# Kernel tuning notes

Measured on AMD Instinct MI355X. Metric: run time of the kernel, lower is better.

The kernel has to match this reference:

```python
import jax, jax.numpy as jnp
from jax import lax
import numpy as np

EPS = 1e-6
D_KQ = 256  # per-head q/k dim; softmax scale = sqrt(256) = 16


def layernorm(x, g, b):
    m = jnp.mean(x, axis=-1, keepdims=True)
    v = jnp.var(x, axis=-1, keepdims=True)  # biased, matches torch LayerNorm
    return (x - m) / jnp.sqrt(v + EPS) * g + b


def lrelu(t):
    return jnp.where(t > 0, t, 0.1 * t)


def setup_inputs() -> dict:
    key = jax.random.key(0)
    ks = jax.random.split(key, 10)
    B, C, H, W = 256, 17, 84, 84
    d_model, heads = 512, 4
    hid = D_KQ * heads  # 1024
    out_dim = 256
    s = 0.05
    return {
        "x": jax.random.normal(ks[0], (B, C, H, W), jnp.float32),
        "conv1_w": jax.random.normal(ks[1], (64, C, 8, 8), jnp.float32) * s,
        "conv1_b": jnp.zeros((64,), jnp.float32),
        "conv2_w": jax.random.normal(ks[2], (510, 64, 4, 4), jnp.float32) * s,
        "conv2_b": jnp.zeros((510,), jnp.float32),
        "wq": jax.random.normal(ks[3], (hid, d_model), jnp.float32) * s,
        "wk": jax.random.normal(ks[4], (hid, d_model), jnp.float32) * s,
        "wv": jax.random.normal(ks[5], (hid, d_model), jnp.float32) * s,
        "ln_e_g": jnp.ones((hid,), jnp.float32),
        "ln_e_b": jnp.zeros((hid,), jnp.float32),
        "wo": jax.random.normal(ks[6], (d_model, hid), jnp.float32) * s,
        "ln_g": jnp.ones((d_model,), jnp.float32),
        "ln_b": jnp.zeros((d_model,), jnp.float32),
        "map_w": jax.random.normal(ks[7], (out_dim, d_model), jnp.float32) * s,
        "map_b": jnp.zeros((out_dim,), jnp.float32),
    }


def reference(x, conv1_w, conv1_b, conv2_w, conv2_b, wq, wk, wv,
              ln_e_g, ln_e_b, wo, ln_g, ln_b, map_w, map_b):
    dn = ("NCHW", "OIHW", "NCHW")
    # feature extractor
    y = lax.conv_general_dilated(x, conv1_w, (4, 4), "VALID", dimension_numbers=dn)
    y = lrelu(y + conv1_b[None, :, None, None])
    y = lax.conv_general_dilated(y, conv2_w, (2, 2), "VALID", dimension_numbers=dn)
    y = lrelu(y + conv2_b[None, :, None, None])  # [B,510,H2,W2]
    B, Cc, H2, W2 = y.shape
    N = H2 * W2
    e = jnp.transpose(y.reshape(B, Cc, N), (0, 2, 1))  # [B,N,510]
    # coordinate augmentation: [(i//W)/H, (i%W)/W]
    idx = jnp.arange(N)
    coord = jnp.stack([(idx // W2) / H2, (idx % W2) / W2], axis=-1).astype(e.dtype)
    e = jnp.concatenate([e, jnp.broadcast_to(coord, (B, N, 2))], axis=-1)  # [B,N,512]
    heads = 4
    # projections + per-projection LayerNorm over full hid dim (pre-head-split)
    q = layernorm(e @ wq.T, ln_e_g, ln_e_b).reshape(B, N, heads, D_KQ)
    k = layernorm(e @ wk.T, ln_e_g, ln_e_b).reshape(B, N, heads, D_KQ)
    v = layernorm(e @ wv.T, ln_e_g, ln_e_b).reshape(B, N, heads, D_KQ)
    scores = jnp.einsum("bnhd,bmhd->bhnm", q, k) / jnp.sqrt(jnp.float32(D_KQ))
    w = jax.nn.softmax(scores, axis=-1)
    nv = jnp.einsum("bhnm,bmhd->bnhd", w, v).reshape(B, N, heads * D_KQ)
    out = layernorm(nv @ wo.T + e, ln_g, ln_b)  # residual + LN
    out = jax.nn.relu(out)
    out = jnp.max(out, axis=1)  # maxout over entities -> [B,512]
    return lrelu(out @ map_w.T + map_b)  # mapping -> [B,256]
```

## Files before the change

kernel.cpp:

```cpp
#include <hip/hip_runtime.h>
#include <hip/hip_bf16.h>
#include <math.h>

typedef __hip_bfloat16 bf16;
using f32x4 = __attribute__((ext_vector_type(4))) float;
using s16x8 = __attribute__((ext_vector_type(8))) short;

#define DEV_INLINE __device__ __forceinline__

static constexpr int BB   = 256;
static constexpr int CIN  = 17;
static constexpr int WIN  = 84;
static constexpr int C1   = 64;
static constexpr int W1   = 20;
static constexpr int P1   = W1 * W1;
static constexpr int C2   = 510;
static constexpr int W2   = 9;
static constexpr int NE   = 81;
static constexpr int DM   = 512;
static constexpr int HID  = 1024;
static constexpr int NH   = 4;
static constexpr int DK   = 256;
static constexpr int MR   = BB * NE;
static constexpr int ODIM = 256;
static constexpr int PLANE = WIN * WIN;
static constexpr int QS   = 3 * HID;

DEV_INLINE float lrelu_f(float v) { return v > 0.f ? v : 0.1f * v; }
DEV_INLINE float bf2f(ushort u) { return __uint_as_float((unsigned)u << 16); }
DEV_INLINE short f2bs(float f) { bf16 t = __float2bfloat16(f); return *reinterpret_cast<short*>(&t); }

DEV_INLINE void gll16(const void* g, const void* l) {
    __builtin_amdgcn_global_load_lds(
        (const __attribute__((address_space(1))) unsigned int*)g,
        (__attribute__((address_space(3))) unsigned int*)l, 16, 0, 0);
}
DEV_INLINE f32x4 mfma16(s16x8 a, s16x8 b, f32x4 c) {
    return __builtin_amdgcn_mfma_f32_16x16x32_bf16(a, b, c, 0, 0, 0);
}

__global__ void k_cast4(const float* __restrict__ s, bf16* __restrict__ d, int n4) {
    const int i4 = blockIdx.x * 256 + threadIdx.x;
    if (i4 >= n4) return;
    const size_t i = (size_t)i4 * 4;
    const float4 v = *(const float4*)(s + i);
    short o[4] = { f2bs(v.x), f2bs(v.y), f2bs(v.z), f2bs(v.w) };
    *(ushort4*)(d + i) = *(ushort4*)o;
}
__global__ void k_castw2(const float* __restrict__ s, bf16* __restrict__ d) {
    const int i = blockIdx.x * 256 + threadIdx.x;
    const int n = i >> 10, rem = i & 1023;
    const int khkw = rem >> 6, ic = rem & 63;
    d[i] = (n < C2) ? __float2bfloat16(s[n * 1024 + ic * 16 + khkw])
                    : __float2bfloat16(0.f);
}
__global__ void k_padb2(const float* __restrict__ s, float* __restrict__ d) {
    const int i = blockIdx.x * 256 + threadIdx.x;
    if (i < 512) d[i] = (i < C2) ? s[i] : 0.f;
}
__global__ void k_castqkv(const float* __restrict__ wq, const float* __restrict__ wk,
                          const float* __restrict__ wv, bf16* __restrict__ d) {
    const int i4 = blockIdx.x * 256 + threadIdx.x;
    const size_t i = (size_t)i4 * 4;
    const int n = (int)(i >> 9), c = (int)(i & 511);
    const float* src = (n < 1024) ? wq : (n < 2048) ? wk : wv;
    const int r = n & 1023;
    const float4 v = *(const float4*)(src + (size_t)r * 512 + c);
    short o[4] = { f2bs(v.x), f2bs(v.y), f2bs(v.z), f2bs(v.w) };
    *(ushort4*)(d + i) = *(ushort4*)o;
}

__global__ __launch_bounds__(512, 1) void k_conv1_mfma(const float* __restrict__ x,
        const bf16* __restrict__ w1b, const float* __restrict__ bias,
        bf16* __restrict__ y1t) {
    __shared__ __align__(16) char pl[2][28224];
    const int b = blockIdx.x;
    const int tid = threadIdx.x;
    const int w = tid >> 6, l = tid & 63;
    const int l15 = l & 15, l4 = l >> 4;
    const float* xb = x + (size_t)b * CIN * PLANE;

    int baseA[4], tval[4];
    #pragma unroll
    for (int j = 0; j < 4; ++j) {
        const int t = w + 8 * j; tval[j] = t;
        int p = t * 16 + l15; if (t >= 25) p = 0;
        const int oh = p / 20, ow = p % 20;
        baseA[j] = (oh * 4 + l4) * 336 + ow * 16;
    }
    float bias_r[4];
    #pragma unroll
    for (int nt = 0; nt < 4; ++nt) bias_r[nt] = bias[nt * 16 + l15];

    #pragma unroll
    for (int it = 0; it < 4; ++it) {
        const int g = it * 512 + tid;
        if (g < 1764) gll16(xb + (size_t)g * 4, pl[0] + (size_t)g * 16);
    }
    __syncthreads();

    f32x4 acc[4][4] = {};
    int cur = 0;
    for (int ic = 0; ic < CIN; ++ic) {
        if (ic + 1 < CIN) {
            const float* src = xb + (size_t)(ic + 1) * PLANE;
            #pragma unroll
            for (int it = 0; it < 4; ++it) {
                const int g = it * 512 + tid;
                if (g < 1764) gll16(src + (size_t)g * 4, pl[cur ^ 1] + (size_t)g * 16);
            }
        }
        s16x8 bq[4][2];
        #pragma unroll
        for (int nt = 0; nt < 4; ++nt)
            #pragma unroll
            for (int ks = 0; ks < 2; ++ks)
                bq[nt][ks] = *(const s16x8*)(w1b + (size_t)(nt * 16 + l15) * 1088
                                             + ic * 64 + (ks * 4 + l4) * 8);
        const char* P = pl[cur];
        #pragma unroll
        for (int j = 0; j < 4; ++j) {
            if (tval[j] < 25) {
                #pragma unroll
                for (int ks = 0; ks < 2; ++ks) {
                    const float* fp = (const float*)(P + baseA[j] + ks * 1344);
                    const f32x4 f0 = *(const f32x4*)fp;
                    const f32x4 f1 = *(const f32x4*)(fp + 4);
                    s16x8 af;
                    #pragma unroll
                    for (int jj = 0; jj < 4; ++jj) {
                        af[jj]     = f2bs(f0[jj]);
                        af[jj + 4] = f2bs(f1[jj]);
                    }
                    #pragma unroll
                    for (int nt = 0; nt < 4; ++nt)
                        acc[j][nt] = mfma16(af, bq[nt][ks], acc[j][nt]);
                }
            }
        }
        __syncthreads();
        cur ^= 1;
    }
    #pragma unroll
    for (int j = 0; j < 4; ++j) {
        if (tval[j] < 25) {
            #pragma unroll
            for (int nt = 0; nt < 4; ++nt) {
                #pragma unroll
                for (int q = 0; q < 4; ++q) {
                    const int pix = tval[j] * 16 + l4 * 4 + q;
                    const int oc  = nt * 16 + l15;
                    y1t[((size_t)b * P1 + pix) * 64 + oc] =
                        __float2bfloat16(lrelu_f(acc[j][nt][q] + bias_r[nt]));
                }
            }
        }
    }
}

__global__ __launch_bounds__(256) void k_gemm_conv2(const bf16* __restrict__ A,
        const bf16* __restrict__ B, const float* __restrict__ bias,
        bf16* __restrict__ Cb) {
    __shared__ __align__(16) char Asm[2][128 * 64];
    __shared__ __align__(16) char Bsm[2][128 * 64];
    const int tid = threadIdx.x;
    const int m0 = blockIdx.y * 128, n0 = blockIdx.x * 128;
    const int w = tid >> 6, l = tid & 63;
    const int wm = w >> 1, wn = w & 1;
    const int l15 = l & 15, l4 = l >> 4;
    const int r0 = tid >> 2, p0 = tid & 3;
    const int r1 = 64 + r0;
    const int sw0 = (p0 ^ ((r0 >> 1) & 3)) << 3;
    const int sw1 = (p0 ^ ((r1 >> 1) & 3)) << 3;
    int bimg[2], ohh[2], oww[2];
    #pragma unroll
    for (int it = 0; it < 2; ++it) {
        const int m = m0 + (it ? r1 : r0);
        bimg[it] = m / 81;
        const int n = m - bimg[it] * 81;
        ohh[it] = n / 9; oww[it] = n - ohh[it] * 9;
    }
    auto stage = [&](int buf, int k0) {
        const int khkw = k0 >> 6, icb = k0 & 63;
        const int kh = khkw >> 2, kwv = khkw & 3;
        const int pix0 = (ohh[0] * 2 + kh) * 20 + oww[0] * 2 + kwv;
        const int pix1 = (ohh[1] * 2 + kh) * 20 + oww[1] * 2 + kwv;
        gll16(A + ((size_t)bimg[0] * P1 + pix0) * 64 + icb + sw0, Asm[buf] + tid * 16);
        gll16(A + ((size_t)bimg[1] * P1 + pix1) * 64 + icb + sw1, Asm[buf] + (256 + tid) * 16);
        gll16(B + (size_t)(n0 + r0) * HID + k0 + sw0, Bsm[buf] + tid * 16);
        gll16(B + (size_t)(n0 + r1) * HID + k0 + sw1, Bsm[buf] + (256 + tid) * 16);
    };
    stage(0, 0);
    __syncthreads();
    f32x4 acc[4][4] = {};
    int cur = 0;
    for (int t = 0; t < 32; ++t) {
        if (t < 31) stage(cur ^ 1, (t + 1) * 32);
        s16x8 af[4], bfv[4];
        #pragma unroll
        for (int i = 0; i < 4; ++i) {
            const int ra = wm * 64 + i * 16 + l15;
            af[i]  = *(const s16x8*)(Asm[cur] + ra * 64 + ((l4 ^ ((ra >> 1) & 3)) << 4));
            const int rb = wn * 64 + i * 16 + l15;
            bfv[i] = *(const s16x8*)(Bsm[cur] + rb * 64 + ((l4 ^ ((rb >> 1) & 3)) << 4));
        }
        #pragma unroll
        for (int i = 0; i < 4; ++i)
            #pragma unroll
            for (int j = 0; j < 4; ++j)
                acc[i][j] = mfma16(af[i], bfv[j], acc[i][j]);
        __syncthreads();
        cur ^= 1;
    }
    #pragma unroll
    for (int i = 0; i < 4; ++i) {
        #pragma unroll
        for (int j = 0; j < 4; ++j) {
            const int col = n0 + wn * 64 + j * 16 + l15;
            #pragma unroll
            for (int q = 0; q < 4; ++q) {
                const int row = m0 + wm * 64 + i * 16 + l4 * 4 + q;
                float v = lrelu_f(acc[i][j][q] + bias[col]);
                if (col >= 510) {
                    const int n = row % 81;
                    v = (col == 510) ? (float)(n / 9) * (1.f / 9.f)
                                     : (float)(n % 9) * (1.f / 9.f);
                }
                Cb[(size_t)row * DM + col] = __float2bfloat16(v);
            }
        }
    }
}

template <int RESID>
__global__ __launch_bounds__(256) void k_gemm_stats(const bf16* __restrict__ A,
        const bf16* __restrict__ B, const bf16* __restrict__ resid,
        bf16* __restrict__ Cb, float2* __restrict__ part,
        int K, int ldc, int nPH) {
    __shared__ __align__(16) char Asm[2][16384];
    __shared__ __align__(16) char Bsm[2][16384];
    const int tid = threadIdx.x;
    const int m0 = blockIdx.y * 128, n0 = blockIdx.x * 128;
    const int w = tid >> 6, l = tid & 63;
    const int wm = w >> 1, wn = w & 1;
    const int l15 = l & 15, l4 = l >> 4;

    auto stage = [&](int buf, int k0) {
        #pragma unroll
        for (int it = 0; it < 4; ++it) {
            const int g = it * 256 + tid;
            const int r = g >> 3, p = g & 7;
            const int sw = (p ^ (r & 7)) << 3;
            gll16(A + (size_t)(m0 + r) * K + k0 + sw, Asm[buf] + g * 16);
            gll16(B + (size_t)(n0 + r) * K + k0 + sw, Bsm[buf] + g * 16);
        }
    };
    stage(0, 0);
    __syncthreads();
    f32x4 acc[4][4] = {};
    int cur = 0;
    const int nt = K >> 6;
    for (int t = 0; t < nt; ++t) {
        if (t + 1 < nt) stage(cur ^ 1, (t + 1) * 64);
        #pragma unroll
        for (int kk = 0; kk < 2; ++kk) {
            s16x8 af[4], bfv[4];
            const int pz = kk * 4 + l4;
            #pragma unroll
            for (int i = 0; i < 4; ++i) {
                const int ra = wm * 64 + i * 16 + l15;
                af[i]  = *(const s16x8*)(Asm[cur] + ra * 128 + ((pz ^ (ra & 7)) << 4));
                const int rb = wn * 64 + i * 16 + l15;
                bfv[i] = *(const s16x8*)(Bsm[cur] + rb * 128 + ((pz ^ (rb & 7)) << 4));
            }
            #pragma unroll
            for (int i = 0; i < 4; ++i)
                #pragma unroll
                for (int j = 0; j < 4; ++j)
                    acc[i][j] = mfma16(af[i], bfv[j], acc[i][j]);
        }
        __syncthreads();
        cur ^= 1;
    }
    #pragma unroll
    for (int i = 0; i < 4; ++i) {
        #pragma unroll
        for (int q = 0; q < 4; ++q) {
            const int row = m0 + wm * 64 + i * 16 + l4 * 4 + q;
            if (RESID) {
                const bf16* rr = resid + (size_t)row * ldc;
                #pragma unroll
                for (int j = 0; j < 4; ++j)
                    acc[i][j][q] += bf2f(*(const ushort*)(rr + n0 + wn * 64 + j * 16 + l15));
            }
            float s = 0.f, s2 = 0.f;
            #pragma unroll
            for (int j = 0; j < 4; ++j) {
                const float v = acc[i][j][q];
                s += v; s2 += v * v;
            }
            #pragma unroll
            for (int o = 1; o < 16; o <<= 1) {
                s  += __shfl_xor(s, o, 64);
                s2 += __shfl_xor(s2, o, 64);
            }
            if (l15 == 0)
                part[(size_t)row * nPH + (n0 >> 6) + wn] = make_float2(s, s2);
            bf16* cr = Cb + (size_t)row * ldc + n0 + wn * 64;
            #pragma unroll
            for (int j = 0; j < 4; ++j)
                cr[j * 16 + l15] = __float2bfloat16(acc[i][j][q]);
        }
    }
}

__global__ void k_red(const float2* __restrict__ part, float2* __restrict__ stats,
                      int total, int nPH, int groups, float invD) {
    const int gid = blockIdx.x * 256 + threadIdx.x;
    if (gid >= total) return;
    const int proj = gid / MR, row = gid - proj * MR;
    const float2* p = part + (size_t)row * (nPH * groups) + proj * nPH;
    float s = 0.f, s2 = 0.f;
    for (int h = 0; h < nPH; ++h) { s += p[h].x; s2 += p[h].y; }
    const float mean = s * invD;
    const float var  = s2 * invD - mean * mean;
    stats[gid] = make_float2(mean, rsqrtf(var + 1e-6f));
}

__global__ __launch_bounds__(256) void k_vt(const bf16* __restrict__ qkv3,
        const float2* __restrict__ vstats, const float* __restrict__ g,
        const float* __restrict__ bprm, bf16* __restrict__ vt) {
    __shared__ bf16 T[81 * 264];
    const int tid = threadIdx.x;
    const int bh = blockIdx.x;
    const int b = bh >> 2, h = bh & 3;
    const int brow = b * NE;
    const int hoff = h * DK;
    for (int gidx = tid; gidx < 81 * 32; gidx += 256) {
        const int m = gidx >> 5, c8 = gidx & 31;
        const int row = brow + m;
        const s16x8 vv = *(const s16x8*)(qkv3 + (size_t)row * QS + 2048 + hoff + c8 * 8);
        const float2 st = vstats[row];
        const int col0 = hoff + c8 * 8;
        const float4 g0 = *(const float4*)(g + col0), g1 = *(const float4*)(g + col0 + 4);
        const float4 b0 = *(const float4*)(bprm + col0), b1 = *(const float4*)(bprm + col0 + 4);
        const float ga[8] = { g0.x, g0.y, g0.z, g0.w, g1.x, g1.y, g1.z, g1.w };
        const float ba[8] = { b0.x, b0.y, b0.z, b0.w, b1.x, b1.y, b1.z, b1.w };
        short o[8];
        #pragma unroll
        for (int jj = 0; jj < 8; ++jj) {
            const float a = st.y * ga[jj];
            o[jj] = f2bs(bf2f((ushort)vv[jj]) * a + (ba[jj] - st.x * a));
        }
        *(s16x8*)(T + m * 264 + c8 * 8) = *(s16x8*)o;
    }
    __syncthreads();
    const int d = tid;
    bf16 row[96];
    #pragma unroll
    for (int m = 0; m < 81; ++m) row[m] = T[m * 264 + d];
    #pragma unroll
    for (int m = 81; m < 96; ++m) row[m] = __float2bfloat16(0.f);
    bf16* out = vt + ((size_t)bh * DK + d) * 96;
    #pragma unroll
    for (int g8 = 0; g8 < 12; ++g8)
        *(s16x8*)(out + g8 * 8) = *(const s16x8*)(&row[g8 * 8]);
}

__global__ __launch_bounds__(512) void k_attn3(const bf16* __restrict__ qkv3,
        const float2* __restrict__ stats, const float* __restrict__ g,
        const float* __restrict__ bprm, const bf16* __restrict__ vt,
        bf16* __restrict__ nv) {
    __shared__ __align__(16) char smem[49152 + 96 * 104 * 2];
    char* Ks = smem;
    bf16* Pb = (bf16*)(smem + 49152);
    const int tid = threadIdx.x;
    const int bh = blockIdx.x;
    const int b = bh >> 2, h = bh & 3;
    const int brow = b * NE;
    const int hoff = h * DK;
    const int w = tid >> 6, l = tid & 63;
    const int l15 = l & 15, l4 = l >> 4;

    for (int gidx = tid; gidx < 96 * 32; gidx += 512) {
        const int r = gidx >> 5, c8 = gidx & 31;
        int krow = brow + r; if (krow >= MR) krow = MR - 1;
        const s16x8 kv = *(const s16x8*)(qkv3 + (size_t)krow * QS + 1024 + hoff + c8 * 8);
        const float2 st = stats[MR + krow];
        const int col0 = hoff + c8 * 8;
        const float4 g0 = *(const float4*)(g + col0), g1 = *(const float4*)(g + col0 + 4);
        const float4 b0 = *(const float4*)(bprm + col0), b1 = *(const float4*)(bprm + col0 + 4);
        const float ga[8] = { g0.x, g0.y, g0.z, g0.w, g1.x, g1.y, g1.z, g1.w };
        const float ba[8] = { b0.x, b0.y, b0.z, b0.w, b1.x, b1.y, b1.z, b1.w };
        short o[8];
        #pragma unroll
        for (int jj = 0; jj < 8; ++jj) {
            const float a = st.y * ga[jj];
            o[jj] = f2bs(bf2f((ushort)kv[jj]) * a + (ba[jj] - st.x * a));
        }
        *(s16x8*)(Ks + r * 512 + ((c8 ^ (r & 7)) << 4)) = *(s16x8*)o;
    }
    __syncthreads();

    if (w < 6) {
        int qrow = brow + w * 16 + l15; if (qrow >= MR) qrow = MR - 1;
        const float2 stq = stats[qrow];
        s16x8 qa[8];
        #pragma unroll
        for (int kk = 0; kk < 8; ++kk) {
            const int col0 = hoff + kk * 32 + l4 * 8;
            const s16x8 qv = *(const s16x8*)(qkv3 + (size_t)qrow * QS + col0);
            const float4 g0 = *(const float4*)(g + col0), g1 = *(const float4*)(g + col0 + 4);
            const float4 b0 = *(const float4*)(bprm + col0), b1 = *(const float4*)(bprm + col0 + 4);
            const float ga[8] = { g0.x, g0.y, g0.z, g0.w, g1.x, g1.y, g1.z, g1.w };
            const float ba[8] = { b0.x, b0.y, b0.z, b0.w, b1.x, b1.y, b1.z, b1.w };
            short o[8];
            #pragma unroll
            for (int jj = 0; jj < 8; ++jj) {
                const float a = stq.y * ga[jj];
                o[jj] = f2bs(bf2f((ushort)qv[jj]) * a + (ba[jj] - stq.x * a));
            }
            qa[kk] = *(s16x8*)o;
        }
        f32x4 sacc[6];
        #pragma unroll
        for (int j = 0; j < 6; ++j) {
            f32x4 a = {};
            const int rb = j * 16 + l15;
            #pragma unroll
            for (int kk = 0; kk < 8; ++kk) {
                const s16x8 kf = *(const s16x8*)(Ks + rb * 512 + (((kk * 4 + l4) ^ (rb & 7)) << 4));
                a = mfma16(qa[kk], kf, a);
            }
            sacc[j] = a;
        }
        float px[6][4];
        #pragma unroll
        for (int q = 0; q < 4; ++q) {
            float m = -1e30f;
            #pragma unroll
            for (int j = 0; j < 6; ++j) {
                const int key = j * 16 + l15;
                const float v = (key < NE) ? sacc[j][q] : -1e30f;
                px[j][q] = v;
                m = fmaxf(m, v);
            }
            #pragma unroll
            for (int o = 1; o < 16; o <<= 1) m = fmaxf(m, __shfl_xor(m, o, 64));
            float s = 0.f;
            #pragma unroll
            for (int j = 0; j < 6; ++j) {
                const float e = __expf((px[j][q] - m) * 0.0625f);
                px[j][q] = e; s += e;
            }
            #pragma unroll
            for (int o = 1; o < 16; o <<= 1) s += __shfl_xor(s, o, 64);
            const float r = 1.f / s;
            #pragma unroll
            for (int j = 0; j < 6; ++j) px[j][q] *= r;
        }
        #pragma unroll
        for (int j = 0; j < 6; ++j)
            #pragma unroll
            for (int q = 0; q < 4; ++q)
                Pb[(w * 16 + l4 * 4 + q) * 104 + j * 16 + l15] =
                    __float2bfloat16(px[j][q]);
    }
    __syncthreads();

    const bf16* vtb = vt + (size_t)bh * DK * 96;
    s16x8 vf[2][3];
    #pragma unroll
    for (int dj = 0; dj < 2; ++dj) {
        const int d = (2 * w + dj) * 16 + l15;
        #pragma unroll
        for (int ks = 0; ks < 3; ++ks)
            vf[dj][ks] = *(const s16x8*)(vtb + (size_t)d * 96 + (ks * 4 + l4) * 8);
    }
    f32x4 oacc[6][2] = {};
    #pragma unroll
    for (int i = 0; i < 6; ++i) {
        s16x8 pa[3];
        #pragma unroll
        for (int ks = 0; ks < 3; ++ks)
            pa[ks] = *(const s16x8*)(Pb + (i * 16 + l15) * 104 + (ks * 4 + l4) * 8);
        #pragma unroll
        for (int dj = 0; dj < 2; ++dj)
            #pragma unroll
            for (int ks = 0; ks < 3; ++ks)
                oacc[i][dj] = mfma16(pa[ks], vf[dj][ks], oacc[i][dj]);
    }
    #pragma unroll
    for (int i = 0; i < 6; ++i) {
        #pragma unroll
        for (int q = 0; q < 4; ++q) {
            const int n = i * 16 + l4 * 4 + q;
            if (n < NE) {
                #pragma unroll
                for (int dj = 0; dj < 2; ++dj) {
                    const int d = (2 * w + dj) * 16 + l15;
                    nv[(size_t)(brow + n) * HID + hoff + d] =
                        __float2bfloat16(oacc[i][dj][q]);
                }
            }
        }
    }
}

__global__ void k_maxpool_ln(const bf16* __restrict__ X, const float2* __restrict__ st,
        const float* __restrict__ g, const float* __restrict__ bprm,
        float* __restrict__ P) {
    const int i = blockIdx.x * 256 + threadIdx.x;
    const int bb = i >> 9, c = i & 511;
    const float gc = g[c], bc = bprm[c];
    const bf16* xp = X + (size_t)bb * NE * DM + c;
    const float2* sp = st + (size_t)bb * NE;
    float mx = -1e30f;
    for (int n = 0; n < NE; ++n) {
        const float2 s = sp[n];
        const float a = s.y * gc;
        const float v = __bfloat162float(xp[(size_t)n * DM]) * a + (bc - s.x * a);
        mx = fmaxf(mx, fmaxf(v, 0.f));
    }
    P[i] = mx;
}

__global__ __launch_bounds__(256) void k_final(const float* __restrict__ P,
        const float* __restrict__ W, const float* __restrict__ bias,
        float* __restrict__ out) {
    const int bb = blockIdx.x;
    __shared__ float pr[DM];
    for (int i = threadIdx.x; i < DM; i += 256) pr[i] = P[(size_t)bb * DM + i];
    __syncthreads();
    const int o = threadIdx.x;
    const float4* w4 = (const float4*)(W + (size_t)o * DM);
    float acc = 0.f;
    for (int c4 = 0; c4 < DM / 4; ++c4) {
        const float4 wv = w4[c4];
        acc += wv.x * pr[c4 * 4] + wv.y * pr[c4 * 4 + 1]
             + wv.z * pr[c4 * 4 + 2] + wv.w * pr[c4 * 4 + 3];
    }
    out[(size_t)bb * ODIM + o] = lrelu_f(acc + bias[o]);
}

extern "C" void kernel_launch(void* const* d_in, const int* in_sizes, int n_in,
                              void* d_out, int out_size, void* d_ws, size_t ws_size,
                              hipStream_t stream) {
    const float* x   = (const float*)d_in[0];
    const float* w1  = (const float*)d_in[1];
    const float* b1  = (const float*)d_in[2];
    const float* w2  = (const float*)d_in[3];
    const float* b2  = (const float*)d_in[4];
    const float* wq  = (const float*)d_in[5];
    const float* wk  = (const float*)d_in[6];
    const float* wvv = (const float*)d_in[7];
    const float* lng = (const float*)d_in[8];
    const float* lnb = (const float*)d_in[9];
    const float* wo  = (const float*)d_in[10];
    const float* lg2 = (const float*)d_in[11];
    const float* lb2 = (const float*)d_in[12];
    const float* mw  = (const float*)d_in[13];
    const float* mb  = (const float*)d_in[14];

    char* ws = (char*)d_ws;
    size_t off = 0;
    auto alloc = [&](size_t bytes) {
        void* p = ws + off;
        off = (off + bytes + 255) & ~(size_t)255;
        return p;
    };
    bf16*   y1t   = (bf16*)  alloc((size_t)BB * P1 * 64 * 2);
    bf16*   ebf   = (bf16*)  alloc((size_t)MR * DM * 2);
    bf16*   qkv3  = (bf16*)  alloc((size_t)MR * QS * 2);
    bf16*   vt    = (bf16*)  alloc((size_t)BB * NH * DK * 96 * 2);
    bf16*   nv    = (bf16*)  alloc((size_t)MR * HID * 2);
    bf16*   ao    = (bf16*)  alloc((size_t)MR * DM * 2);
    float*  pool  = (float*) alloc((size_t)BB * DM * 4);
    float2* part1 = (float2*)alloc((size_t)MR * 48 * 8);
    float2* part2 = (float2*)alloc((size_t)MR * 8 * 8);
    float2* stQKV = (float2*)alloc((size_t)3 * MR * 8);
    float2* st2   = (float2*)alloc((size_t)MR * 8);
    bf16*   w1b   = (bf16*)  alloc((size_t)C1 * CIN * 64 * 2);
    bf16*   w2b   = (bf16*)  alloc((size_t)512 * HID * 2);
    float*  b2p   = (float*) alloc(512 * 4);
    bf16*   wqkv  = (bf16*)  alloc((size_t)3072 * DM * 2);
    bf16*   wob   = (bf16*)  alloc((size_t)DM * HID * 2);
    float*  outp  = (float*)d_out;

    k_cast4<<<(C1 * CIN * 64 / 4 + 255) / 256, 256, 0, stream>>>(w1, w1b, C1 * CIN * 64 / 4);
    k_castw2<<<512 * HID / 256, 256, 0, stream>>>(w2, w2b);
    k_padb2<<<2, 256, 0, stream>>>(b2, b2p);
    k_castqkv<<<3072 * DM / 4 / 256, 256, 0, stream>>>(wq, wk, wvv, wqkv);
    k_cast4<<<(DM * HID / 4) / 256, 256, 0, stream>>>(wo, wob, DM * HID / 4);

    k_conv1_mfma<<<BB, 512, 0, stream>>>(x, w1b, b1, y1t);

    k_gemm_conv2<<<dim3(4, MR / 128), 256, 0, stream>>>(y1t, w2b, b2p, ebf);

    k_gemm_stats<0><<<dim3(24, MR / 128), 256, 0, stream>>>(ebf, wqkv, nullptr,
                                                            qkv3, part1, DM, QS, 48);
    k_red<<<(3 * MR + 255) / 256, 256, 0, stream>>>(part1, stQKV, 3 * MR, 16, 3,
                                                    1.f / 1024.f);

    k_vt<<<BB * NH, 256, 0, stream>>>(qkv3, stQKV + 2 * MR, lng, lnb, vt);

    k_attn3<<<BB * NH, 512, 0, stream>>>(qkv3, stQKV, lng, lnb, vt, nv);

    k_gemm_stats<1><<<dim3(4, MR / 128), 256, 0, stream>>>(nv, wob, ebf,
                                                           ao, part2, HID, DM, 8);
    k_red<<<(MR + 255) / 256, 256, 0, stream>>>(part2, st2, MR, 8, 1, 1.f / 512.f);

    k_maxpool_ln<<<(BB * DM) / 256, 256, 0, stream>>>(ao, st2, lg2, lb2, pool);
    k_final<<<BB, 256, 0, stream>>>(pool, mw, mb, outp);
}
```

Before: 390.2 us.

## Fuse weight-prep kernels, remap GEMM blocks across XCDs, use single-buffer K32 GEMM

Merges the five weight-cast launches into one prep kernel to cut launch overhead. The conv2 and stats GEMMs get a 1D grid with an XCD-aware block remap (lin&7 interleave) so neighbouring tiles land on the same chiplet and share L2. The stats GEMM goes from double-buffered K=64 staging to a smaller single-buffered K=32 tile, which lowers LDS use and may raise occupancy but gives up load/compute overlap and adds more barriers per K.

New measurement: 379.9 us. 1.03x faster.

```diff
diff --git a/kernel.cpp b/kernel.cpp
--- a/kernel.cpp
+++ b/kernel.cpp
@@ -39,35 +39,47 @@
     return __builtin_amdgcn_mfma_f32_16x16x32_bf16(a, b, c, 0, 0, 0);
 }
 
-__global__ void k_cast4(const float* __restrict__ s, bf16* __restrict__ d, int n4) {
-    const int i4 = blockIdx.x * 256 + threadIdx.x;
-    if (i4 >= n4) return;
-    const size_t i = (size_t)i4 * 4;
-    const float4 v = *(const float4*)(s + i);
-    short o[4] = { f2bs(v.x), f2bs(v.y), f2bs(v.z), f2bs(v.w) };
-    *(ushort4*)(d + i) = *(ushort4*)o;
-}
-__global__ void k_castw2(const float* __restrict__ s, bf16* __restrict__ d) {
-    const int i = blockIdx.x * 256 + threadIdx.x;
-    const int n = i >> 10, rem = i & 1023;
-    const int khkw = rem >> 6, ic = rem & 63;
-    d[i] = (n < C2) ? __float2bfloat16(s[n * 1024 + ic * 16 + khkw])
-                    : __float2bfloat16(0.f);
-}
-__global__ void k_padb2(const float* __restrict__ s, float* __restrict__ d) {
-    const int i = blockIdx.x * 256 + threadIdx.x;
-    if (i < 512) d[i] = (i < C2) ? s[i] : 0.f;
-}
-__global__ void k_castqkv(const float* __restrict__ wq, const float* __restrict__ wk,
-                          const float* __restrict__ wv, bf16* __restrict__ d) {
-    const int i4 = blockIdx.x * 256 + threadIdx.x;
-    const size_t i = (size_t)i4 * 4;
-    const int n = (int)(i >> 9), c = (int)(i & 511);
-    const float* src = (n < 1024) ? wq : (n < 2048) ? wk : wv;
-    const int r = n & 1023;
-    const float4 v = *(const float4*)(src + (size_t)r * 512 + c);
-    short o[4] = { f2bs(v.x), f2bs(v.y), f2bs(v.z), f2bs(v.w) };
-    *(ushort4*)(d + i) = *(ushort4*)o;
+__global__ void k_prep(const float* __restrict__ w1, const float* __restrict__ w2,
+        const float* __restrict__ b2, const float* __restrict__ wq,
+        const float* __restrict__ wk, const float* __restrict__ wv,
+        const float* __restrict__ wo, bf16* __restrict__ w1b,
+        bf16* __restrict__ w2b, float* __restrict__ b2p,
+        bf16* __restrict__ wqkv, bf16* __restrict__ wob) {
+    int i = blockIdx.x * 256 + threadIdx.x;
+    if (i < 17408) {
+        const size_t o = (size_t)i * 4;
+        const float4 v = *(const float4*)(w1 + o);
+        short r[4] = { f2bs(v.x), f2bs(v.y), f2bs(v.z), f2bs(v.w) };
+        *(ushort4*)(w1b + o) = *(ushort4*)r;
+        return;
+    }
+    i -= 17408;
+    if (i < 524288) {
+        const int n = i >> 10, rem = i & 1023;
+        const int khkw = rem >> 6, ic = rem & 63;
+        w2b[i] = (n < C2) ? __float2bfloat16(w2[n * 1024 + ic * 16 + khkw])
+                          : __float2bfloat16(0.f);
+        return;
+    }
+    i -= 524288;
+    if (i < 512) { b2p[i] = (i < C2) ? b2[i] : 0.f; return; }
+    i -= 512;
+    if (i < 393216) {
+        const size_t o = (size_t)i * 4;
+        const int n = (int)(o >> 9), c = (int)(o & 511);
+        const float* src = (n < 1024) ? wq : (n < 2048) ? wk : wv;
+        const float4 v = *(const float4*)(src + (size_t)(n & 1023) * 512 + c);
+        short r[4] = { f2bs(v.x), f2bs(v.y), f2bs(v.z), f2bs(v.w) };
+        *(ushort4*)(wqkv + o) = *(ushort4*)r;
+        return;
+    }
+    i -= 393216;
+    if (i < 131072) {
+        const size_t o = (size_t)i * 4;
+        const float4 v = *(const float4*)(wo + o);
+        short r[4] = { f2bs(v.x), f2bs(v.y), f2bs(v.z), f2bs(v.w) };
+        *(ushort4*)(wob + o) = *(ushort4*)r;
+    }
 }
 
 __global__ __launch_bounds__(512, 1) void k_conv1_mfma(const float* __restrict__ x,
@@ -164,7 +176,9 @@
     __shared__ __align__(16) char Asm[2][128 * 64];
     __shared__ __align__(16) char Bsm[2][128 * 64];
     const int tid = threadIdx.x;
-    const int m0 = blockIdx.y * 128, n0 = blockIdx.x * 128;
+    int lin = blockIdx.x;
+    lin = (lin & 7) * (gridDim.x >> 3) + (lin >> 3);
+    const int m0 = (lin >> 2) * 128, n0 = (lin & 3) * 128;
     const int w = tid >> 6, l = tid & 63;
     const int wm = w >> 1, wn = w & 1;
     const int l15 = l & 15, l4 = l >> 4;
@@ -233,54 +247,45 @@
 }
 
 template <int RESID>
-__global__ __launch_bounds__(256) void k_gemm_stats(const bf16* __restrict__ A,
+__global__ __launch_bounds__(256) void k_gemm32(const bf16* __restrict__ A,
         const bf16* __restrict__ B, const bf16* __restrict__ resid,
         bf16* __restrict__ Cb, float2* __restrict__ part,
-        int K, int ldc, int nPH) {
-    __shared__ __align__(16) char Asm[2][16384];
-    __shared__ __align__(16) char Bsm[2][16384];
+        int K, int ldc, int nPH, int gx) {
+    __shared__ __align__(16) char Asm[128 * 64];
+    __shared__ __align__(16) char Bsm[128 * 64];
     const int tid = threadIdx.x;
-    const int m0 = blockIdx.y * 128, n0 = blockIdx.x * 128;
+    int lin = blockIdx.x;
+    lin = (lin & 7) * ((int)gridDim.x >> 3) + (lin >> 3);
+    const int bx = lin % gx, by = lin / gx;
+    const int m0 = by * 128, n0 = bx * 128;
     const int w = tid >> 6, l = tid & 63;
     const int wm = w >> 1, wn = w & 1;
     const int l15 = l & 15, l4 = l >> 4;
-
-    auto stage = [&](int buf, int k0) {
-        #pragma unroll
-        for (int it = 0; it < 4; ++it) {
-            const int g = it * 256 + tid;
-            const int r = g >> 3, p = g & 7;
-            const int sw = (p ^ (r & 7)) << 3;
-            gll16(A + (size_t)(m0 + r) * K + k0 + sw, Asm[buf] + g * 16);
-            gll16(B + (size_t)(n0 + r) * K + k0 + sw, Bsm[buf] + g * 16);
-        }
-    };
-    stage(0, 0);
-    __syncthreads();
+    const int r0 = tid >> 2, p0 = tid & 3;
+    const int r1 = 64 + r0;
+    const int sw0 = (p0 ^ ((r0 >> 1) & 3)) << 3;
+    const int sw1 = (p0 ^ ((r1 >> 1) & 3)) << 3;
     f32x4 acc[4][4] = {};
-    int cur = 0;
-    const int nt = K >> 6;
-    for (int t = 0; t < nt; ++t) {
-        if (t + 1 < nt) stage(cur ^ 1, (t + 1) * 64);
-        #pragma unroll
-        for (int kk = 0; kk < 2; ++kk) {
-            s16x8 af[4], bfv[4];
-            const int pz = kk * 4 + l4;
-            #pragma unroll
-            for (int i = 0; i < 4; ++i) {
-                const int ra = wm * 64 + i * 16 + l15;
-                af[i]  = *(const s16x8*)(Asm[cur] + ra * 128 + ((pz ^ (ra & 7)) << 4));
-                const int rb = wn * 64 + i * 16 + l15;
-                bfv[i] = *(const s16x8*)(Bsm[cur] + rb * 128 + ((pz ^ (rb & 7)) << 4));
-            }
-            #pragma unroll
-            for (int i = 0; i < 4; ++i)
-                #pragma unroll
-                for (int j = 0; j < 4; ++j)
-                    acc[i][j] = mfma16(af[i], bfv[j], acc[i][j]);
-        }
+    for (int k0 = 0; k0 < K; k0 += 32) {
+        gll16(A + (size_t)(m0 + r0) * K + k0 + sw0, Asm + tid * 16);
+        gll16(A + (size_t)(m0 + r1) * K + k0 + sw1, Asm + (256 + tid) * 16);
+        gll16(B + (size_t)(n0 + r0) * K + k0 + sw0, Bsm + tid * 16);
+        gll16(B + (size_t)(n0 + r1) * K + k0 + sw1, Bsm + (256 + tid) * 16);
         __syncthreads();
-        cur ^= 1;
+        s16x8 af[4], bfv[4];
+        #pragma unroll
+        for (int i = 0; i < 4; ++i) {
+            const int ra = wm * 64 + i * 16 + l15;
+            af[i]  = *(const s16x8*)(Asm + ra * 64 + ((l4 ^ ((ra >> 1) & 3)) << 4));
+            const int rb = wn * 64 + i * 16 + l15;
+            bfv[i] = *(const s16x8*)(Bsm + rb * 64 + ((l4 ^ ((rb >> 1) & 3)) << 4));
+        }
+        #pragma unroll
+        for (int i = 0; i < 4; ++i)
+            #pragma unroll
+            for (int j = 0; j < 4; ++j)
+                acc[i][j] = mfma16(af[i], bfv[j], acc[i][j]);
+        __syncthreads();
     }
     #pragma unroll
     for (int i = 0; i < 4; ++i) {
@@ -587,18 +592,15 @@
     bf16*   wob   = (bf16*)  alloc((size_t)DM * HID * 2);
     float*  outp  = (float*)d_out;
 
-    k_cast4<<<(C1 * CIN * 64 / 4 + 255) / 256, 256, 0, stream>>>(w1, w1b, C1 * CIN * 64 / 4);
-    k_castw2<<<512 * HID / 256, 256, 0, stream>>>(w2, w2b);
-    k_padb2<<<2, 256, 0, stream>>>(b2, b2p);
-    k_castqkv<<<3072 * DM / 4 / 256, 256, 0, stream>>>(wq, wk, wvv, wqkv);
-    k_cast4<<<(DM * HID / 4) / 256, 256, 0, stream>>>(wo, wob, DM * HID / 4);
+    k_prep<<<4166, 256, 0, stream>>>(w1, w2, b2, wq, wk, wvv, wo,
+                                     w1b, w2b, b2p, wqkv, wob);
 
     k_conv1_mfma<<<BB, 512, 0, stream>>>(x, w1b, b1, y1t);
 
-    k_gemm_conv2<<<dim3(4, MR / 128), 256, 0, stream>>>(y1t, w2b, b2p, ebf);
-
-    k_gemm_stats<0><<<dim3(24, MR / 128), 256, 0, stream>>>(ebf, wqkv, nullptr,
-                                                            qkv3, part1, DM, QS, 48);
+    k_gemm_conv2<<<648, 256, 0, stream>>>(y1t, w2b, b2p, ebf);
+
+    k_gemm32<0><<<3888, 256, 0, stream>>>(ebf, wqkv, nullptr, qkv3, part1,
+                                          DM, QS, 48, 24);
     k_red<<<(3 * MR + 255) / 256, 256, 0, stream>>>(part1, stQKV, 3 * MR, 16, 3,
                                                     1.f / 1024.f);
 
@@ -606,8 +608,8 @@
 
     k_attn3<<<BB * NH, 512, 0, stream>>>(qkv3, stQKV, lng, lnb, vt, nv);
 
-    k_gemm_stats<1><<<dim3(4, MR / 128), 256, 0, stream>>>(nv, wob, ebf,
-                                                           ao, part2, HID, DM, 8);
+    k_gemm32<1><<<648, 256, 0, stream>>>(nv, wob, ebf, ao, part2,
+                                         HID, DM, 8, 4);
     k_red<<<(MR + 255) / 256, 256, 0, stream>>>(part2, st2, MR, 8, 1, 1.f / 512.f);
 
     k_maxpool_ln<<<(BB * DM) / 256, 256, 0, stream>>>(ao, st2, lg2, lb2, pool);
```
